# Performance work log

Hardware: AMD Instinct MI355X
Metric: run time of the kernel (lower is better)

Reference implementation:

```python
import jax, jax.numpy as jnp
import numpy as np

N_HEAD = 16
EMBED = 1024
HEAD_DIM = EMBED // N_HEAD  # 64
HALF = HEAD_DIM // 2        # 32
T = 2048                    # total packed tokens
NSEG = 4
SEG = T // NSEG             # 512 tokens per packed sequence
SCALE = HEAD_DIM ** -0.5


def _apply_rotary_vision(t, freqs):
    # t: [T, H, D], freqs: [T, D/2] -> Qwen2-VL style vision RoPE
    cos = jnp.concatenate([jnp.cos(freqs), jnp.cos(freqs)], axis=-1)[:, None, :]  # [T,1,D]
    sin = jnp.concatenate([jnp.sin(freqs), jnp.sin(freqs)], axis=-1)[:, None, :]
    t1, t2 = t[..., :HALF], t[..., HALF:]
    rot = jnp.concatenate([-t2, t1], axis=-1)  # rotate_half
    return t * cos + rot * sin


def setup_inputs() -> dict:
    key = jax.random.key(0)
    k1, k2, k3, k4, k5 = jax.random.split(key, 5)
    hidden_states = jax.random.normal(k1, (T, EMBED), dtype=jnp.float32)
    cu_seqlens = (jnp.arange(NSEG + 1, dtype=jnp.int32) * SEG)  # [0,512,...,2048]
    # realistic rotary freqs: position within each segment * inverse frequencies
    pos = jnp.tile(jnp.arange(SEG, dtype=jnp.float32), NSEG)  # [T]
    inv_freq = 1.0 / (10000.0 ** (jnp.arange(HALF, dtype=jnp.float32) / HALF))
    rotary_pos_emb = pos[:, None] * inv_freq[None, :]  # [T, HALF]
    std = 0.02
    wq = jax.random.normal(k2, (EMBED, EMBED), dtype=jnp.float32) * std
    wk = jax.random.normal(k3, (EMBED, EMBED), dtype=jnp.float32) * std
    wv = jax.random.normal(k4, (EMBED, EMBED), dtype=jnp.float32) * std
    wo = jax.random.normal(k5, (EMBED, EMBED), dtype=jnp.float32) * std
    return {"hidden_states": hidden_states, "cu_seqlens": cu_seqlens,
            "rotary_pos_emb": rotary_pos_emb, "wq": wq, "wk": wk, "wv": wv, "wo": wo}


def reference(hidden_states, cu_seqlens, rotary_pos_emb, wq, wk, wv, wo):
    # QKV projections (nn.Linear, bias=False): y = x @ W.T
    q = (hidden_states @ wq.T).reshape(T, N_HEAD, HEAD_DIM)
    k = (hidden_states @ wk.T).reshape(T, N_HEAD, HEAD_DIM)
    v = (hidden_states @ wv.T).reshape(T, N_HEAD, HEAD_DIM)
    q = _apply_rotary_vision(q, rotary_pos_emb)
    k = _apply_rotary_vision(k, rotary_pos_emb)
    # varlen (block-diagonal, non-causal) attention over packed segments
    seg_id = jnp.searchsorted(cu_seqlens, jnp.arange(T, dtype=cu_seqlens.dtype), side='right')
    same_seg = seg_id[:, None] == seg_id[None, :]  # [T, T]
    scores = jnp.einsum('thd,shd->hts', q, k) * SCALE  # [H, T, T]
    scores = jnp.where(same_seg[None, :, :], scores, jnp.finfo(scores.dtype).min)
    probs = jax.nn.softmax(scores, axis=-1)
    attn = jnp.einsum('hts,shd->thd', probs, v).reshape(T, EMBED)
    return attn @ wo.T
```

## Files before the change

kernel.cpp:

```cpp
#include <hip/hip_runtime.h>
#include <cstdint>

#define T_TOK 2048
#define EMBED 1024
#define NH    16
#define HD    64
#define HALF  32
#define SEG   512
#define SL    (0.125f * 1.44269504088896f)

typedef __attribute__((ext_vector_type(8))) __bf16 bf16x8;
typedef __attribute__((ext_vector_type(4))) float  f32x4;
typedef unsigned short u16;
typedef unsigned int   u32;

__device__ __forceinline__ u16 f2bf(float f) {
  u32 u = __builtin_bit_cast(u32, f);
  u += 0x7fffu + ((u >> 16) & 1u);
  return (u16)(u >> 16);
}

__device__ __forceinline__ void gld_lds16(const void* g, void* l) {
  __builtin_amdgcn_global_load_lds(
      reinterpret_cast<__attribute__((address_space(1))) u32*>(
          reinterpret_cast<uintptr_t>(g)),
      reinterpret_cast<__attribute__((address_space(3))) u32*>(
          reinterpret_cast<uintptr_t>(l)),
      16, 0, 0);
}

__global__ __launch_bounds__(256) void convert_k(
    const float* __restrict__ H,  const float* __restrict__ wq,
    const float* __restrict__ wk, const float* __restrict__ wv,
    const float* __restrict__ wo, u16* __restrict__ dst) {
  const size_t gid = (size_t)blockIdx.x * 256 + threadIdx.x;
  const size_t e = gid * 4;
  const float* src; size_t off;
  const size_t HN = (size_t)T_TOK * EMBED;
  if (e < HN) { src = H; off = e; }
  else {
    size_t r = e - HN;
    int w = (int)(r >> 20);
    off = r & ((1u << 20) - 1);
    src = (w == 0) ? wq : (w == 1) ? wk : (w == 2) ? wv : wo;
  }
  const float4 v = *(const float4*)(src + off);
  ushort4 o;
  o.x = f2bf(v.x); o.y = f2bf(v.y); o.z = f2bf(v.z); o.w = f2bf(v.w);
  *(ushort4*)(dst + e) = o;
}

template <int MODE>
__global__ __launch_bounds__(256) void gemm_bt(
    const u16* __restrict__ A, const u16* __restrict__ B,
    void* __restrict__ Cv, const float* __restrict__ rope) {
  constexpr int K = 1024, N = 1024;
  __shared__ alignas(16) u16 As[2][2][64 * 32];
  __shared__ alignas(16) u16 Bs[2][2][128 * 32];
  const int tid = threadIdx.x;
  const int wave = tid >> 6, lane = tid & 63;
  const int quad = lane >> 4, l16 = lane & 15;
  const int bm = blockIdx.y * 64, bn = blockIdx.x * 128;
  const u16* Bz = B + ((size_t)blockIdx.z << 20);
  const int wm = (wave >> 1) * 32, wn = (wave & 1) * 64;

  f32x4 acc[2][4];
#pragma unroll
  for (int i = 0; i < 2; ++i)
#pragma unroll
    for (int j = 0; j < 4; ++j) { f32x4 z = {0.f, 0.f, 0.f, 0.f}; acc[i][j] = z; }

  const int srow = tid >> 2, scol = (tid & 3) * 8;
  const u16* gA = A  + (size_t)(bm + srow) * K + scol;
  const u16* gB = Bz + (size_t)(bn + srow) * K + scol;

#pragma unroll
  for (int p = 0; p < 2; ++p) {
    gld_lds16(gA + p * 32, (char*)&As[0][p][0] + wave * 1024);
    gld_lds16(gB + p * 32, (char*)&Bs[0][p][0] + wave * 1024);
    gld_lds16(gB + (size_t)64 * K + p * 32, (char*)&Bs[0][p][64 * 32] + wave * 1024);
  }

  for (int kk = 0; kk < K; kk += 64) {
    __syncthreads();
    const int cur = (kk >> 6) & 1, nxt = cur ^ 1;
    if (kk + 64 < K) {
      const int kn = kk + 64;
#pragma unroll
      for (int p = 0; p < 2; ++p) {
        gld_lds16(gA + kn + p * 32, (char*)&As[nxt][p][0] + wave * 1024);
        gld_lds16(gB + kn + p * 32, (char*)&Bs[nxt][p][0] + wave * 1024);
        gld_lds16(gB + (size_t)64 * K + kn + p * 32,
                  (char*)&Bs[nxt][p][64 * 32] + wave * 1024);
      }
    }
#pragma unroll
    for (int p = 0; p < 2; ++p) {
      const u16* Ac = &As[cur][p][0];
      const u16* Bc = &Bs[cur][p][0];
      bf16x8 af[2], bfv[4];
#pragma unroll
      for (int i = 0; i < 2; ++i)
        af[i] = *(const bf16x8*)(Ac + (wm + i * 16 + l16) * 32 + quad * 8);
#pragma unroll
      for (int j = 0; j < 4; ++j)
        bfv[j] = *(const bf16x8*)(Bc + (wn + j * 16 + l16) * 32 + quad * 8);
#pragma unroll
      for (int i = 0; i < 2; ++i)
#pragma unroll
        for (int j = 0; j < 4; ++j)
          acc[i][j] = __builtin_amdgcn_mfma_f32_16x16x32_bf16(af[i], bfv[j],
                                                              acc[i][j], 0, 0, 0);
    }
  }

  if (MODE == 0) {
    float* C = (float*)Cv;
#pragma unroll
    for (int i = 0; i < 2; ++i)
#pragma unroll
      for (int r = 0; r < 4; ++r) {
        const int row = bm + wm + i * 16 + quad * 4 + r;
#pragma unroll
        for (int j = 0; j < 4; ++j)
          C[(size_t)row * N + bn + wn + j * 16 + l16] = acc[i][j][r];
      }
  } else {
    const int z = blockIdx.z;
    if (z < 2) {
      u16* dst = (u16*)Cv + ((size_t)z << 21);
#pragma unroll
      for (int i = 0; i < 2; ++i)
#pragma unroll
        for (int r = 0; r < 4; ++r) {
          const int t = bm + wm + i * 16 + quad * 4 + r;
          const float f0 = rope[t * HALF + l16];
          const float f1 = rope[t * HALF + 16 + l16];
          float s0, c0, s1, c1;
          __sincosf(f0, &s0, &c0);
          __sincosf(f1, &s1, &c1);
          const float v0 = acc[i][0][r], v1 = acc[i][1][r];
          const float v2 = acc[i][2][r], v3 = acc[i][3][r];
          const size_t base = (size_t)t * N + bn + wn + l16;
          dst[base]      = f2bf(v0 * c0 - v2 * s0);
          dst[base + 16] = f2bf(v1 * c1 - v3 * s1);
          dst[base + 32] = f2bf(v2 * c0 + v0 * s0);
          dst[base + 48] = f2bf(v3 * c1 + v1 * s1);
        }
    } else {
      u16* Vt = (u16*)Cv + ((size_t)2 << 21);
#pragma unroll
      for (int i = 0; i < 2; ++i) {
        const int t0 = bm + wm + i * 16 + quad * 4;
#pragma unroll
        for (int j = 0; j < 4; ++j) {
          const int col = bn + wn + j * 16 + l16;
          ushort4 pk;
          pk.x = f2bf(acc[i][j][0]); pk.y = f2bf(acc[i][j][1]);
          pk.z = f2bf(acc[i][j][2]); pk.w = f2bf(acc[i][j][3]);
          *(ushort4*)(Vt + (size_t)col * T_TOK + t0) = pk;
        }
      }
    }
  }
}

__global__ __launch_bounds__(256) void attn_k(
    const u16* __restrict__ Qb, const u16* __restrict__ Kb,
    const u16* __restrict__ Vt, u16* __restrict__ Ab) {
  const int qt = blockIdx.x, seg = blockIdx.y, h = blockIdx.z;
  const int tid = threadIdx.x;
  const int wave = tid >> 6, lane = tid & 63;
  const int quad = lane >> 4, l16 = lane & 15;

  __shared__ alignas(16) u16 Pl[4 * 16 * 72];

  const int qbase = seg * SEG + qt * 64 + wave * 16;
  const u16* qp = Qb + (size_t)(qbase + l16) * EMBED + h * HD + quad * 8;
  const bf16x8 qf0 = *(const bf16x8*)qp;
  const bf16x8 qf1 = *(const bf16x8*)(qp + 32);

  float mold[4] = {-1e30f, -1e30f, -1e30f, -1e30f};
  float lsum[4] = {0.f, 0.f, 0.f, 0.f};
  f32x4 O[4];
#pragma unroll
  for (int nt = 0; nt < 4; ++nt) { f32x4 z = {0.f, 0.f, 0.f, 0.f}; O[nt] = z; }

  u16* pw = Pl + wave * 1152;

  for (int cc = 0; cc < 8; ++cc) {
    const int c0 = cc * 64;
    f32x4 S[4];
#pragma unroll
    for (int kt = 0; kt < 4; ++kt) {
      const u16* kp = Kb + (size_t)(seg * SEG + c0 + kt * 16 + l16) * EMBED +
                      h * HD + quad * 8;
      bf16x8 kf0 = *(const bf16x8*)kp;
      bf16x8 kf1 = *(const bf16x8*)(kp + 32);
      f32x4 s = {0.f, 0.f, 0.f, 0.f};
      s = __builtin_amdgcn_mfma_f32_16x16x32_bf16(qf0, kf0, s, 0, 0, 0);
      s = __builtin_amdgcn_mfma_f32_16x16x32_bf16(qf1, kf1, s, 0, 0, 0);
      S[kt] = s;
    }
    bf16x8 vf0[4], vf1[4];
#pragma unroll
    for (int nt = 0; nt < 4; ++nt) {
      const u16* vp = Vt + (size_t)(h * HD + nt * 16 + l16) * T_TOK +
                      seg * SEG + c0 + quad * 8;
      vf0[nt] = *(const bf16x8*)vp;
      vf1[nt] = *(const bf16x8*)(vp + 32);
    }
    float mx[4], al[4];
#pragma unroll
    for (int r = 0; r < 4; ++r) {
      float m = fmaxf(fmaxf(S[0][r], S[1][r]), fmaxf(S[2][r], S[3][r]));
#pragma unroll
      for (int off = 1; off < 16; off <<= 1) m = fmaxf(m, __shfl_xor(m, off));
      float mn = fmaxf(mold[r], m);
      al[r] = exp2f((mold[r] - mn) * SL);
      mold[r] = mn;
      mx[r] = mn;
    }
    float ps[4] = {0.f, 0.f, 0.f, 0.f};
#pragma unroll
    for (int kt = 0; kt < 4; ++kt)
#pragma unroll
      for (int r = 0; r < 4; ++r) {
        float p = exp2f((S[kt][r] - mx[r]) * SL);
        ps[r] += p;
        pw[(quad * 4 + r) * 72 + kt * 16 + l16] = f2bf(p);
      }
#pragma unroll
    for (int r = 0; r < 4; ++r) lsum[r] = lsum[r] * al[r] + ps[r];
#pragma unroll
    for (int nt = 0; nt < 4; ++nt) {
      O[nt][0] *= al[0]; O[nt][1] *= al[1];
      O[nt][2] *= al[2]; O[nt][3] *= al[3];
    }
    const u16* pp = pw + l16 * 72 + quad * 8;
    bf16x8 pf0 = *(const bf16x8*)pp;
    bf16x8 pf1 = *(const bf16x8*)(pp + 32);
#pragma unroll
    for (int nt = 0; nt < 4; ++nt) {
      O[nt] = __builtin_amdgcn_mfma_f32_16x16x32_bf16(pf0, vf0[nt], O[nt], 0, 0, 0);
      O[nt] = __builtin_amdgcn_mfma_f32_16x16x32_bf16(pf1, vf1[nt], O[nt], 0, 0, 0);
    }
  }
#pragma unroll
  for (int r = 0; r < 4; ++r) {
    float l = lsum[r];
#pragma unroll
    for (int off = 1; off < 16; off <<= 1) l += __shfl_xor(l, off);
    lsum[r] = 1.f / l;
  }
#pragma unroll
  for (int nt = 0; nt < 4; ++nt)
#pragma unroll
    for (int r = 0; r < 4; ++r) {
      const int trow = qbase + quad * 4 + r;
      Ab[(size_t)trow * EMBED + h * HD + nt * 16 + l16] = f2bf(O[nt][r] * lsum[r]);
    }
}

extern "C" void kernel_launch(void* const* d_in, const int* in_sizes, int n_in,
                              void* d_out, int out_size, void* d_ws,
                              size_t ws_size, hipStream_t stream) {
  const float* H    = (const float*)d_in[0];
  const float* rope = (const float*)d_in[2];
  const float* wq   = (const float*)d_in[3];
  const float* wk   = (const float*)d_in[4];
  const float* wv   = (const float*)d_in[5];
  const float* wo   = (const float*)d_in[6];

  constexpr size_t M1 = (size_t)1 << 20;
  if (ws_size < 28 * M1) return;

  u16* ws16 = (u16*)d_ws;
  u16* Hb = ws16;
  u16* Wb = ws16 + 2 * M1;
  u16* Qb = ws16 + 6 * M1;
  u16* Kb = ws16 + 8 * M1;
  u16* Vt = ws16 + 10 * M1;
  u16* Ab = ws16 + 12 * M1;

  convert_k<<<6144, 256, 0, stream>>>(H, wq, wk, wv, wo, ws16);
  gemm_bt<1><<<dim3(8, 32, 3), 256, 0, stream>>>(Hb, Wb, (void*)Qb, rope);
  attn_k<<<dim3(8, 4, 16), 256, 0, stream>>>(Qb, Kb, Vt, Ab);
  gemm_bt<0><<<dim3(8, 32, 1), 256, 0, stream>>>(Ab, Wb + 3 * M1, d_out, nullptr);
}
```

Before: 152.7 us.

## Replace LDS-staged GEMMs with direct global-to-register MFMA loads and larger QKV tiles

Both projection GEMMs now load bf16 fragments straight from global memory into registers with a two-stage register prefetch, instead of staging tiles through LDS with global_load_lds and block barriers. The QKV GEMM tile grows from 64x128 to 128x128, so each wave holds 4x4 accumulators and the grid shrinks. The attention launch is flattened to a 1D grid with a different block ordering. This removes LDS traffic and __syncthreads, but each wave now reads its own fragments from global memory without sharing them through LDS, so there is more redundant global/L2 traffic and higher register pressure.

Measured after the change: 203.6 us. 1.33x slower.

```diff
diff --git a/kernel.cpp b/kernel.cpp
--- a/kernel.cpp
+++ b/kernel.cpp
@@ -18,15 +18,6 @@
   u32 u = __builtin_bit_cast(u32, f);
   u += 0x7fffu + ((u >> 16) & 1u);
   return (u16)(u >> 16);
-}
-
-__device__ __forceinline__ void gld_lds16(const void* g, void* l) {
-  __builtin_amdgcn_global_load_lds(
-      reinterpret_cast<__attribute__((address_space(1))) u32*>(
-          reinterpret_cast<uintptr_t>(g)),
-      reinterpret_cast<__attribute__((address_space(3))) u32*>(
-          reinterpret_cast<uintptr_t>(l)),
-      16, 0, 0);
 }
 
 __global__ __launch_bounds__(256) void convert_k(
@@ -50,125 +41,149 @@
   *(ushort4*)(dst + e) = o;
 }
 
-template <int MODE>
-__global__ __launch_bounds__(256) void gemm_bt(
+template <int WM>
+__device__ __forceinline__ void gemm_core(
     const u16* __restrict__ A, const u16* __restrict__ B,
-    void* __restrict__ Cv, const float* __restrict__ rope) {
-  constexpr int K = 1024, N = 1024;
-  __shared__ alignas(16) u16 As[2][2][64 * 32];
-  __shared__ alignas(16) u16 Bs[2][2][128 * 32];
+    int bm, int bn, int wm, int wn, int quad, int l16,
+    f32x4 (&acc)[WM][4]) {
+  constexpr int K = 1024;
+  const u16* pa = A + (size_t)(bm + wm + l16) * K + quad * 8;
+  const u16* pb = B + (size_t)(bn + wn + l16) * K + quad * 8;
+
+  bf16x8 aF[2][WM], bF[2][4];
+#pragma unroll
+  for (int i = 0; i < WM; ++i) {
+    aF[0][i] = *(const bf16x8*)(pa + (size_t)i * 16 * K);
+    aF[1][i] = *(const bf16x8*)(pa + (size_t)i * 16 * K + 32);
+  }
+#pragma unroll
+  for (int j = 0; j < 4; ++j) {
+    bF[0][j] = *(const bf16x8*)(pb + (size_t)j * 16 * K);
+    bF[1][j] = *(const bf16x8*)(pb + (size_t)j * 16 * K + 32);
+  }
+
+  for (int kk = 0; kk < K; kk += 64) {
+#pragma unroll
+    for (int i = 0; i < WM; ++i)
+#pragma unroll
+      for (int j = 0; j < 4; ++j)
+        acc[i][j] = __builtin_amdgcn_mfma_f32_16x16x32_bf16(aF[0][i], bF[0][j],
+                                                            acc[i][j], 0, 0, 0);
+    if (kk + 64 < K) {
+#pragma unroll
+      for (int i = 0; i < WM; ++i)
+        aF[0][i] = *(const bf16x8*)(pa + (size_t)i * 16 * K + kk + 64);
+#pragma unroll
+      for (int j = 0; j < 4; ++j)
+        bF[0][j] = *(const bf16x8*)(pb + (size_t)j * 16 * K + kk + 64);
+    }
+#pragma unroll
+    for (int i = 0; i < WM; ++i)
+#pragma unroll
+      for (int j = 0; j < 4; ++j)
+        acc[i][j] = __builtin_amdgcn_mfma_f32_16x16x32_bf16(aF[1][i], bF[1][j],
+                                                            acc[i][j], 0, 0, 0);
+    if (kk + 96 < K) {
+#pragma unroll
+      for (int i = 0; i < WM; ++i)
+        aF[1][i] = *(const bf16x8*)(pa + (size_t)i * 16 * K + kk + 96);
+#pragma unroll
+      for (int j = 0; j < 4; ++j)
+        bF[1][j] = *(const bf16x8*)(pb + (size_t)j * 16 * K + kk + 96);
+    }
+  }
+}
+
+__global__ __launch_bounds__(256) void qkv_direct(
+    const u16* __restrict__ Hb, const u16* __restrict__ Wb,
+    const float* __restrict__ rope, u16* __restrict__ Qb,
+    u16* __restrict__ Kb, u16* __restrict__ Vt) {
+  constexpr int N = 1024;
+  const int tid = threadIdx.x;
+  const int wave = tid >> 6, lane = tid & 63;
+  const int quad = lane >> 4, l16 = lane & 15;
+  const int bm = blockIdx.y * 128, bn = blockIdx.x * 128;
+  const int wm = (wave >> 1) * 64, wn = (wave & 1) * 64;
+  const int z = blockIdx.z;
+
+  f32x4 acc[4][4];
+#pragma unroll
+  for (int i = 0; i < 4; ++i)
+#pragma unroll
+    for (int j = 0; j < 4; ++j) { f32x4 zz = {0.f, 0.f, 0.f, 0.f}; acc[i][j] = zz; }
+
+  gemm_core<4>(Hb, Wb + ((size_t)z << 20), bm, bn, wm, wn, quad, l16, acc);
+
+  if (z < 2) {
+    u16* dst = z ? Kb : Qb;
+#pragma unroll
+    for (int i = 0; i < 4; ++i)
+#pragma unroll
+      for (int r = 0; r < 4; ++r) {
+        const int t = bm + wm + i * 16 + quad * 4 + r;
+        const float f0 = rope[t * HALF + l16];
+        const float f1 = rope[t * HALF + 16 + l16];
+        float s0, c0, s1, c1;
+        __sincosf(f0, &s0, &c0);
+        __sincosf(f1, &s1, &c1);
+        const float v0 = acc[i][0][r], v1 = acc[i][1][r];
+        const float v2 = acc[i][2][r], v3 = acc[i][3][r];
+        const size_t base = (size_t)t * N + bn + wn + l16;
+        dst[base]      = f2bf(v0 * c0 - v2 * s0);
+        dst[base + 16] = f2bf(v1 * c1 - v3 * s1);
+        dst[base + 32] = f2bf(v2 * c0 + v0 * s0);
+        dst[base + 48] = f2bf(v3 * c1 + v1 * s1);
+      }
+  } else {
+#pragma unroll
+    for (int i = 0; i < 4; ++i) {
+      const int t0 = bm + wm + i * 16 + quad * 4;
+#pragma unroll
+      for (int j = 0; j < 4; ++j) {
+        const int col = bn + wn + j * 16 + l16;
+        ushort4 pk;
+        pk.x = f2bf(acc[i][j][0]); pk.y = f2bf(acc[i][j][1]);
+        pk.z = f2bf(acc[i][j][2]); pk.w = f2bf(acc[i][j][3]);
+        *(ushort4*)(Vt + (size_t)col * T_TOK + t0) = pk;
+      }
+    }
+  }
+}
+
+__global__ __launch_bounds__(256) void oproj_direct(
+    const u16* __restrict__ Ab, const u16* __restrict__ Wo,
+    float* __restrict__ out) {
+  constexpr int N = 1024;
   const int tid = threadIdx.x;
   const int wave = tid >> 6, lane = tid & 63;
   const int quad = lane >> 4, l16 = lane & 15;
   const int bm = blockIdx.y * 64, bn = blockIdx.x * 128;
-  const u16* Bz = B + ((size_t)blockIdx.z << 20);
   const int wm = (wave >> 1) * 32, wn = (wave & 1) * 64;
 
   f32x4 acc[2][4];
 #pragma unroll
   for (int i = 0; i < 2; ++i)
 #pragma unroll
-    for (int j = 0; j < 4; ++j) { f32x4 z = {0.f, 0.f, 0.f, 0.f}; acc[i][j] = z; }
-
-  const int srow = tid >> 2, scol = (tid & 3) * 8;
-  const u16* gA = A  + (size_t)(bm + srow) * K + scol;
-  const u16* gB = Bz + (size_t)(bn + srow) * K + scol;
-
-#pragma unroll
-  for (int p = 0; p < 2; ++p) {
-    gld_lds16(gA + p * 32, (char*)&As[0][p][0] + wave * 1024);
-    gld_lds16(gB + p * 32, (char*)&Bs[0][p][0] + wave * 1024);
-    gld_lds16(gB + (size_t)64 * K + p * 32, (char*)&Bs[0][p][64 * 32] + wave * 1024);
-  }
-
-  for (int kk = 0; kk < K; kk += 64) {
-    __syncthreads();
-    const int cur = (kk >> 6) & 1, nxt = cur ^ 1;
-    if (kk + 64 < K) {
-      const int kn = kk + 64;
-#pragma unroll
-      for (int p = 0; p < 2; ++p) {
-        gld_lds16(gA + kn + p * 32, (char*)&As[nxt][p][0] + wave * 1024);
-        gld_lds16(gB + kn + p * 32, (char*)&Bs[nxt][p][0] + wave * 1024);
-        gld_lds16(gB + (size_t)64 * K + kn + p * 32,
-                  (char*)&Bs[nxt][p][64 * 32] + wave * 1024);
-      }
-    }
-#pragma unroll
-    for (int p = 0; p < 2; ++p) {
-      const u16* Ac = &As[cur][p][0];
-      const u16* Bc = &Bs[cur][p][0];
-      bf16x8 af[2], bfv[4];
-#pragma unroll
-      for (int i = 0; i < 2; ++i)
-        af[i] = *(const bf16x8*)(Ac + (wm + i * 16 + l16) * 32 + quad * 8);
-#pragma unroll
-      for (int j = 0; j < 4; ++j)
-        bfv[j] = *(const bf16x8*)(Bc + (wn + j * 16 + l16) * 32 + quad * 8);
-#pragma unroll
-      for (int i = 0; i < 2; ++i)
-#pragma unroll
-        for (int j = 0; j < 4; ++j)
-          acc[i][j] = __builtin_amdgcn_mfma_f32_16x16x32_bf16(af[i], bfv[j],
-                                                              acc[i][j], 0, 0, 0);
-    }
-  }
-
-  if (MODE == 0) {
-    float* C = (float*)Cv;
-#pragma unroll
-    for (int i = 0; i < 2; ++i)
-#pragma unroll
-      for (int r = 0; r < 4; ++r) {
-        const int row = bm + wm + i * 16 + quad * 4 + r;
-#pragma unroll
-        for (int j = 0; j < 4; ++j)
-          C[(size_t)row * N + bn + wn + j * 16 + l16] = acc[i][j][r];
-      }
-  } else {
-    const int z = blockIdx.z;
-    if (z < 2) {
-      u16* dst = (u16*)Cv + ((size_t)z << 21);
-#pragma unroll
-      for (int i = 0; i < 2; ++i)
-#pragma unroll
-        for (int r = 0; r < 4; ++r) {
-          const int t = bm + wm + i * 16 + quad * 4 + r;
-          const float f0 = rope[t * HALF + l16];
-          const float f1 = rope[t * HALF + 16 + l16];
-          float s0, c0, s1, c1;
-          __sincosf(f0, &s0, &c0);
-          __sincosf(f1, &s1, &c1);
-          const float v0 = acc[i][0][r], v1 = acc[i][1][r];
-          const float v2 = acc[i][2][r], v3 = acc[i][3][r];
-          const size_t base = (size_t)t * N + bn + wn + l16;
-          dst[base]      = f2bf(v0 * c0 - v2 * s0);
-          dst[base + 16] = f2bf(v1 * c1 - v3 * s1);
-          dst[base + 32] = f2bf(v2 * c0 + v0 * s0);
-          dst[base + 48] = f2bf(v3 * c1 + v1 * s1);
-        }
-    } else {
-      u16* Vt = (u16*)Cv + ((size_t)2 << 21);
-#pragma unroll
-      for (int i = 0; i < 2; ++i) {
-        const int t0 = bm + wm + i * 16 + quad * 4;
-#pragma unroll
-        for (int j = 0; j < 4; ++j) {
-          const int col = bn + wn + j * 16 + l16;
-          ushort4 pk;
-          pk.x = f2bf(acc[i][j][0]); pk.y = f2bf(acc[i][j][1]);
-          pk.z = f2bf(acc[i][j][2]); pk.w = f2bf(acc[i][j][3]);
-          *(ushort4*)(Vt + (size_t)col * T_TOK + t0) = pk;
-        }
-      }
-    }
-  }
+    for (int j = 0; j < 4; ++j) { f32x4 zz = {0.f, 0.f, 0.f, 0.f}; acc[i][j] = zz; }
+
+  gemm_core<2>(Ab, Wo, bm, bn, wm, wn, quad, l16, acc);
+
+#pragma unroll
+  for (int i = 0; i < 2; ++i)
+#pragma unroll
+    for (int r = 0; r < 4; ++r) {
+      const int row = bm + wm + i * 16 + quad * 4 + r;
+#pragma unroll
+      for (int j = 0; j < 4; ++j)
+        out[(size_t)row * N + bn + wn + j * 16 + l16] = acc[i][j][r];
+    }
 }
 
 __global__ __launch_bounds__(256) void attn_k(
     const u16* __restrict__ Qb, const u16* __restrict__ Kb,
     const u16* __restrict__ Vt, u16* __restrict__ Ab) {
-  const int qt = blockIdx.x, seg = blockIdx.y, h = blockIdx.z;
+  const int b = blockIdx.x;
+  const int qt = b & 7, seg = (b >> 3) & 3, h = b >> 5;
   const int tid = threadIdx.x;
   const int wave = tid >> 6, lane = tid & 63;
   const int quad = lane >> 4, l16 = lane & 15;
@@ -271,6 +286,7 @@
   const float* wk   = (const float*)d_in[4];
   const float* wv   = (const float*)d_in[5];
   const float* wo   = (const float*)d_in[6];
+  float* out        = (float*)d_out;
 
   constexpr size_t M1 = (size_t)1 << 20;
   if (ws_size < 28 * M1) return;
@@ -284,7 +300,7 @@
   u16* Ab = ws16 + 12 * M1;
 
   convert_k<<<6144, 256, 0, stream>>>(H, wq, wk, wv, wo, ws16);
-  gemm_bt<1><<<dim3(8, 32, 3), 256, 0, stream>>>(Hb, Wb, (void*)Qb, rope);
-  attn_k<<<dim3(8, 4, 16), 256, 0, stream>>>(Qb, Kb, Vt, Ab);
-  gemm_bt<0><<<dim3(8, 32, 1), 256, 0, stream>>>(Ab, Wb + 3 * M1, d_out, nullptr);
-}
+  qkv_direct<<<dim3(8, 16, 3), 256, 0, stream>>>(Hb, Wb, rope, Qb, Kb, Vt);
+  attn_k<<<512, 256, 0, stream>>>(Qb, Kb, Vt, Ab);
+  oproj_direct<<<dim3(8, 32), 256, 0, stream>>>(Ab, Wb + 3 * M1, out);
+}
```

## Fuse Q projection and RoPE into attention kernel, split KV projection

Applied to the files above, without the earlier changes.

Moves the Q projection and its rotary embedding into the attention kernel. Each wave computes its 16x64 Q tile directly from global memory with MFMA, applies RoPE, and stages the result through LDS. The K/V projection becomes its own kernel with one fewer z-slice, and the output projection becomes a dedicated kernel. This removes the Q write and read-back round trip through global memory. In exchange, the attention kernel does a K=1024 GEMM with unshared, non-LDS global loads, and the Wq head slice is reloaded once per query tile.

Result: slower. 174.2 us (+14.1%).

```diff
diff --git a/kernel.cpp b/kernel.cpp
--- a/kernel.cpp
+++ b/kernel.cpp
@@ -50,10 +50,10 @@
   *(ushort4*)(dst + e) = o;
 }
 
-template <int MODE>
-__global__ __launch_bounds__(256) void gemm_bt(
-    const u16* __restrict__ A, const u16* __restrict__ B,
-    void* __restrict__ Cv, const float* __restrict__ rope) {
+__global__ __launch_bounds__(256) void kvproj_k(
+    const u16* __restrict__ Hb, const u16* __restrict__ Wb,
+    const float* __restrict__ rope, u16* __restrict__ Kb,
+    u16* __restrict__ Vt) {
   constexpr int K = 1024, N = 1024;
   __shared__ alignas(16) u16 As[2][2][64 * 32];
   __shared__ alignas(16) u16 Bs[2][2][128 * 32];
@@ -61,7 +61,7 @@
   const int wave = tid >> 6, lane = tid & 63;
   const int quad = lane >> 4, l16 = lane & 15;
   const int bm = blockIdx.y * 64, bn = blockIdx.x * 128;
-  const u16* Bz = B + ((size_t)blockIdx.z << 20);
+  const u16* Bz = Wb + ((size_t)(blockIdx.z + 1) << 20);
   const int wm = (wave >> 1) * 32, wn = (wave & 1) * 64;
 
   f32x4 acc[2][4];
@@ -71,7 +71,7 @@
     for (int j = 0; j < 4; ++j) { f32x4 z = {0.f, 0.f, 0.f, 0.f}; acc[i][j] = z; }
 
   const int srow = tid >> 2, scol = (tid & 3) * 8;
-  const u16* gA = A  + (size_t)(bm + srow) * K + scol;
+  const u16* gA = Hb + (size_t)(bm + srow) * K + scol;
   const u16* gB = Bz + (size_t)(bn + srow) * K + scol;
 
 #pragma unroll
@@ -114,71 +114,115 @@
     }
   }
 
-  if (MODE == 0) {
-    float* C = (float*)Cv;
+  if (blockIdx.z == 0) {
 #pragma unroll
     for (int i = 0; i < 2; ++i)
 #pragma unroll
       for (int r = 0; r < 4; ++r) {
-        const int row = bm + wm + i * 16 + quad * 4 + r;
-#pragma unroll
-        for (int j = 0; j < 4; ++j)
-          C[(size_t)row * N + bn + wn + j * 16 + l16] = acc[i][j][r];
+        const int t = bm + wm + i * 16 + quad * 4 + r;
+        const float f0 = rope[t * HALF + l16];
+        const float f1 = rope[t * HALF + 16 + l16];
+        float s0, c0, s1, c1;
+        __sincosf(f0, &s0, &c0);
+        __sincosf(f1, &s1, &c1);
+        const float v0 = acc[i][0][r], v1 = acc[i][1][r];
+        const float v2 = acc[i][2][r], v3 = acc[i][3][r];
+        const size_t base = (size_t)t * N + bn + wn + l16;
+        Kb[base]      = f2bf(v0 * c0 - v2 * s0);
+        Kb[base + 16] = f2bf(v1 * c1 - v3 * s1);
+        Kb[base + 32] = f2bf(v2 * c0 + v0 * s0);
+        Kb[base + 48] = f2bf(v3 * c1 + v1 * s1);
       }
   } else {
-    const int z = blockIdx.z;
-    if (z < 2) {
-      u16* dst = (u16*)Cv + ((size_t)z << 21);
-#pragma unroll
-      for (int i = 0; i < 2; ++i)
-#pragma unroll
-        for (int r = 0; r < 4; ++r) {
-          const int t = bm + wm + i * 16 + quad * 4 + r;
-          const float f0 = rope[t * HALF + l16];
-          const float f1 = rope[t * HALF + 16 + l16];
-          float s0, c0, s1, c1;
-          __sincosf(f0, &s0, &c0);
-          __sincosf(f1, &s1, &c1);
-          const float v0 = acc[i][0][r], v1 = acc[i][1][r];
-          const float v2 = acc[i][2][r], v3 = acc[i][3][r];
-          const size_t base = (size_t)t * N + bn + wn + l16;
-          dst[base]      = f2bf(v0 * c0 - v2 * s0);
-          dst[base + 16] = f2bf(v1 * c1 - v3 * s1);
-          dst[base + 32] = f2bf(v2 * c0 + v0 * s0);
-          dst[base + 48] = f2bf(v3 * c1 + v1 * s1);
-        }
-    } else {
-      u16* Vt = (u16*)Cv + ((size_t)2 << 21);
-#pragma unroll
-      for (int i = 0; i < 2; ++i) {
-        const int t0 = bm + wm + i * 16 + quad * 4;
-#pragma unroll
-        for (int j = 0; j < 4; ++j) {
-          const int col = bn + wn + j * 16 + l16;
-          ushort4 pk;
-          pk.x = f2bf(acc[i][j][0]); pk.y = f2bf(acc[i][j][1]);
-          pk.z = f2bf(acc[i][j][2]); pk.w = f2bf(acc[i][j][3]);
-          *(ushort4*)(Vt + (size_t)col * T_TOK + t0) = pk;
-        }
-      }
-    }
-  }
-}
-
-__global__ __launch_bounds__(256) void attn_k(
-    const u16* __restrict__ Qb, const u16* __restrict__ Kb,
+#pragma unroll
+    for (int i = 0; i < 2; ++i) {
+      const int t0 = bm + wm + i * 16 + quad * 4;
+#pragma unroll
+      for (int j = 0; j < 4; ++j) {
+        const int col = bn + wn + j * 16 + l16;
+        ushort4 pk;
+        pk.x = f2bf(acc[i][j][0]); pk.y = f2bf(acc[i][j][1]);
+        pk.z = f2bf(acc[i][j][2]); pk.w = f2bf(acc[i][j][3]);
+        *(ushort4*)(Vt + (size_t)col * T_TOK + t0) = pk;
+      }
+    }
+  }
+}
+
+__global__ __launch_bounds__(256) void qattn_k(
+    const u16* __restrict__ Hb, const u16* __restrict__ Wq,
+    const float* __restrict__ rope, const u16* __restrict__ Kb,
     const u16* __restrict__ Vt, u16* __restrict__ Ab) {
-  const int qt = blockIdx.x, seg = blockIdx.y, h = blockIdx.z;
+  const int b = blockIdx.x;
+  const int qt = b & 7, seg = (b >> 3) & 3, h = b >> 5;
   const int tid = threadIdx.x;
   const int wave = tid >> 6, lane = tid & 63;
   const int quad = lane >> 4, l16 = lane & 15;
 
   __shared__ alignas(16) u16 Pl[4 * 16 * 72];
+  __shared__ alignas(16) u16 Ql[4 * 16 * 72];
 
   const int qbase = seg * SEG + qt * 64 + wave * 16;
-  const u16* qp = Qb + (size_t)(qbase + l16) * EMBED + h * HD + quad * 8;
-  const bf16x8 qf0 = *(const bf16x8*)qp;
-  const bf16x8 qf1 = *(const bf16x8*)(qp + 32);
+
+  f32x4 qa[4];
+#pragma unroll
+  for (int j = 0; j < 4; ++j) { f32x4 z = {0.f, 0.f, 0.f, 0.f}; qa[j] = z; }
+  {
+    constexpr int K = 1024;
+    const u16* pa = Hb + (size_t)(qbase + l16) * K + quad * 8;
+    const u16* pb = Wq + (size_t)(h * HD + l16) * K + quad * 8;
+    bf16x8 aF[2], bF[2][4];
+    aF[0] = *(const bf16x8*)pa;
+    aF[1] = *(const bf16x8*)(pa + 32);
+#pragma unroll
+    for (int j = 0; j < 4; ++j) {
+      bF[0][j] = *(const bf16x8*)(pb + (size_t)j * 16 * K);
+      bF[1][j] = *(const bf16x8*)(pb + (size_t)j * 16 * K + 32);
+    }
+    for (int kk = 0; kk < K; kk += 64) {
+#pragma unroll
+      for (int j = 0; j < 4; ++j)
+        qa[j] = __builtin_amdgcn_mfma_f32_16x16x32_bf16(aF[0], bF[0][j],
+                                                        qa[j], 0, 0, 0);
+      if (kk + 64 < K) {
+        aF[0] = *(const bf16x8*)(pa + kk + 64);
+#pragma unroll
+        for (int j = 0; j < 4; ++j)
+          bF[0][j] = *(const bf16x8*)(pb + (size_t)j * 16 * K + kk + 64);
+      }
+#pragma unroll
+      for (int j = 0; j < 4; ++j)
+        qa[j] = __builtin_amdgcn_mfma_f32_16x16x32_bf16(aF[1], bF[1][j],
+                                                        qa[j], 0, 0, 0);
+      if (kk + 96 < K) {
+        aF[1] = *(const bf16x8*)(pa + kk + 96);
+#pragma unroll
+        for (int j = 0; j < 4; ++j)
+          bF[1][j] = *(const bf16x8*)(pb + (size_t)j * 16 * K + kk + 96);
+      }
+    }
+  }
+
+  u16* qlw = Ql + wave * 1152;
+#pragma unroll
+  for (int r = 0; r < 4; ++r) {
+    const int t = qbase + quad * 4 + r;
+    const float f0 = rope[t * HALF + l16];
+    const float f1 = rope[t * HALF + 16 + l16];
+    float s0, c0, s1, c1;
+    __sincosf(f0, &s0, &c0);
+    __sincosf(f1, &s1, &c1);
+    const float v0 = qa[0][r], v1 = qa[1][r];
+    const float v2 = qa[2][r], v3 = qa[3][r];
+    const int row = quad * 4 + r;
+    qlw[row * 72 + l16]      = f2bf(v0 * c0 - v2 * s0);
+    qlw[row * 72 + 16 + l16] = f2bf(v1 * c1 - v3 * s1);
+    qlw[row * 72 + 32 + l16] = f2bf(v2 * c0 + v0 * s0);
+    qlw[row * 72 + 48 + l16] = f2bf(v3 * c1 + v1 * s1);
+  }
+  const u16* qrp = qlw + l16 * 72 + quad * 8;
+  const bf16x8 qf0 = *(const bf16x8*)qrp;
+  const bf16x8 qf1 = *(const bf16x8*)(qrp + 32);
 
   float mold[4] = {-1e30f, -1e30f, -1e30f, -1e30f};
   float lsum[4] = {0.f, 0.f, 0.f, 0.f};
@@ -262,6 +306,79 @@
     }
 }
 
+__global__ __launch_bounds__(256) void oproj_k(
+    const u16* __restrict__ Ab, const u16* __restrict__ Wo,
+    float* __restrict__ out) {
+  constexpr int K = 1024, N = 1024;
+  __shared__ alignas(16) u16 As[2][2][64 * 32];
+  __shared__ alignas(16) u16 Bs[2][2][128 * 32];
+  const int tid = threadIdx.x;
+  const int wave = tid >> 6, lane = tid & 63;
+  const int quad = lane >> 4, l16 = lane & 15;
+  const int bm = blockIdx.y * 64, bn = blockIdx.x * 128;
+  const int wm = (wave >> 1) * 32, wn = (wave & 1) * 64;
+
+  f32x4 acc[2][4];
+#pragma unroll
+  for (int i = 0; i < 2; ++i)
+#pragma unroll
+    for (int j = 0; j < 4; ++j) { f32x4 z = {0.f, 0.f, 0.f, 0.f}; acc[i][j] = z; }
+
+  const int srow = tid >> 2, scol = (tid & 3) * 8;
+  const u16* gA = Ab + (size_t)(bm + srow) * K + scol;
+  const u16* gB = Wo + (size_t)(bn + srow) * K + scol;
+
+#pragma unroll
+  for (int p = 0; p < 2; ++p) {
+    gld_lds16(gA + p * 32, (char*)&As[0][p][0] + wave * 1024);
+    gld_lds16(gB + p * 32, (char*)&Bs[0][p][0] + wave * 1024);
+    gld_lds16(gB + (size_t)64 * K + p * 32, (char*)&Bs[0][p][64 * 32] + wave * 1024);
+  }
+
+  for (int kk = 0; kk < K; kk += 64) {
+    __syncthreads();
+    const int cur = (kk >> 6) & 1, nxt = cur ^ 1;
+    if (kk + 64 < K) {
+      const int kn = kk + 64;
+#pragma unroll
+      for (int p = 0; p < 2; ++p) {
+        gld_lds16(gA + kn + p * 32, (char*)&As[nxt][p][0] + wave * 1024);
+        gld_lds16(gB + kn + p * 32, (char*)&Bs[nxt][p][0] + wave * 1024);
+        gld_lds16(gB + (size_t)64 * K + kn + p * 32,
+                  (char*)&Bs[nxt][p][64 * 32] + wave * 1024);
+      }
+    }
+#pragma unroll
+    for (int p = 0; p < 2; ++p) {
+      const u16* Ac = &As[cur][p][0];
+      const u16* Bc = &Bs[cur][p][0];
+      bf16x8 af[2], bfv[4];
+#pragma unroll
+      for (int i = 0; i < 2; ++i)
+        af[i] = *(const bf16x8*)(Ac + (wm + i * 16 + l16) * 32 + quad * 8);
+#pragma unroll
+      for (int j = 0; j < 4; ++j)
+        bfv[j] = *(const bf16x8*)(Bc + (wn + j * 16 + l16) * 32 + quad * 8);
+#pragma unroll
+      for (int i = 0; i < 2; ++i)
+#pragma unroll
+        for (int j = 0; j < 4; ++j)
+          acc[i][j] = __builtin_amdgcn_mfma_f32_16x16x32_bf16(af[i], bfv[j],
+                                                              acc[i][j], 0, 0, 0);
+    }
+  }
+
+#pragma unroll
+  for (int i = 0; i < 2; ++i)
+#pragma unroll
+    for (int r = 0; r < 4; ++r) {
+      const int row = bm + wm + i * 16 + quad * 4 + r;
+#pragma unroll
+      for (int j = 0; j < 4; ++j)
+        out[(size_t)row * N + bn + wn + j * 16 + l16] = acc[i][j][r];
+    }
+}
+
 extern "C" void kernel_launch(void* const* d_in, const int* in_sizes, int n_in,
                               void* d_out, int out_size, void* d_ws,
                               size_t ws_size, hipStream_t stream) {
@@ -271,6 +388,7 @@
   const float* wk   = (const float*)d_in[4];
   const float* wv   = (const float*)d_in[5];
   const float* wo   = (const float*)d_in[6];
+  float* out        = (float*)d_out;
 
   constexpr size_t M1 = (size_t)1 << 20;
   if (ws_size < 28 * M1) return;
@@ -278,13 +396,12 @@
   u16* ws16 = (u16*)d_ws;
   u16* Hb = ws16;
   u16* Wb = ws16 + 2 * M1;
-  u16* Qb = ws16 + 6 * M1;
   u16* Kb = ws16 + 8 * M1;
   u16* Vt = ws16 + 10 * M1;
   u16* Ab = ws16 + 12 * M1;
 
   convert_k<<<6144, 256, 0, stream>>>(H, wq, wk, wv, wo, ws16);
-  gemm_bt<1><<<dim3(8, 32, 3), 256, 0, stream>>>(Hb, Wb, (void*)Qb, rope);
-  attn_k<<<dim3(8, 4, 16), 256, 0, stream>>>(Qb, Kb, Vt, Ab);
-  gemm_bt<0><<<dim3(8, 32, 1), 256, 0, stream>>>(Ab, Wb + 3 * M1, d_out, nullptr);
-}
+  kvproj_k<<<dim3(8, 32, 2), 256, 0, stream>>>(Hb, Wb, rope, Kb, Vt);
+  qattn_k<<<512, 256, 0, stream>>>(Hb, Wb , rope, Kb, Vt, Ab);
+  oproj_k<<<dim3(8, 32), 256, 0, stream>>>(Ab, Wb + 3 * M1, out);
+}
```
